# Performance work log

Hardware: AMD Instinct MI355X
Metric: run time of the kernel (lower is better)

Reference implementation:

```python
import jax, jax.numpy as jnp
import numpy as np

AUDIO_DIM, SEM_DIM, ATTN_DIM = 512, 768, 128


def setup_inputs() -> dict:
    key = jax.random.key(0)
    ks = jax.random.split(key, 12)
    B, T, T_sem = 8, 4096, 1024
    s = lambda d: 1.0 / np.sqrt(d)
    return {
        "x_ct": jax.random.normal(ks[0], (B, AUDIO_DIM, T), jnp.float32),
        "sem_btd": jax.random.normal(ks[1], (B, T_sem, SEM_DIM), jnp.float32),
        "ln_w": jnp.ones((AUDIO_DIM,), jnp.float32),
        "ln_b": jnp.zeros((AUDIO_DIM,), jnp.float32),
        "Wq": jax.random.normal(ks[2], (AUDIO_DIM, ATTN_DIM), jnp.float32) * s(AUDIO_DIM),
        "bq": jnp.zeros((ATTN_DIM,), jnp.float32),
        "Wk": jax.random.normal(ks[3], (SEM_DIM, ATTN_DIM), jnp.float32) * s(SEM_DIM),
        "bk": jnp.zeros((ATTN_DIM,), jnp.float32),
        "Wv": jax.random.normal(ks[4], (SEM_DIM, ATTN_DIM), jnp.float32) * s(SEM_DIM),
        "bv": jnp.zeros((ATTN_DIM,), jnp.float32),
        "Wo": jax.random.normal(ks[5], (ATTN_DIM, AUDIO_DIM), jnp.float32) * s(ATTN_DIM),
        "bo": jnp.zeros((AUDIO_DIM,), jnp.float32),
    }


def _layernorm(x, w, b, eps=1e-5):
    mu = jnp.mean(x, axis=-1, keepdims=True)
    var = jnp.mean(jnp.square(x - mu), axis=-1, keepdims=True)
    return (x - mu) * jax.lax.rsqrt(var + eps) * w + b


def reference(x_ct, sem_btd, ln_w, ln_b, Wq, bq, Wk, bk, Wv, bv, Wo, bo):
    # x_ct: [B, C, T] -> [B, T, C]
    x = jnp.swapaxes(x_ct, 1, 2)
    x = _layernorm(x, ln_w, ln_b)
    Q = x @ Wq + bq                      # [B, T, A]
    K = sem_btd @ Wk + bk                # [B, S, A]
    V = sem_btd @ Wv + bv                # [B, S, A]
    scale = ATTN_DIM ** -0.5
    attn = jnp.einsum("bta,bsa->bts", Q, K) * scale
    attn = jax.nn.softmax(attn, axis=-1)  # dropout: eval mode (identity)
    ctx = jnp.einsum("bts,bsa->bta", attn, V)
    delta = ctx @ Wo + bo                # [B, T, C]
    return jnp.swapaxes(delta, 1, 2)     # [B, C, T]
```

## Files before the change

### kernel.cpp

```cpp
#include <hip/hip_runtime.h>
#include <hip/hip_bf16.h>
#include <math.h>

#define BATCH 8
#define TDIM 4096
#define SDIM 1024
#define CDIM 512
#define DDIM 768
#define ADIM 128

typedef short s8v __attribute__((ext_vector_type(8)));
typedef float f4v __attribute__((ext_vector_type(4)));

__device__ __forceinline__ short f2bf(float f) {
    unsigned u = __float_as_uint(f);
    u += 0x7fffu + ((u >> 16) & 1u);
    return (short)(u >> 16);
}
__device__ __forceinline__ float bf2f(short s) {
    return __uint_as_float(((unsigned)(unsigned short)s) << 16);
}
__device__ __forceinline__ f4v mfma16(s8v a, s8v b, f4v c) {
    return __builtin_amdgcn_mfma_f32_16x16x32_bf16(a, b, c, 0, 0, 0);
}
__device__ __forceinline__ void gl_lds16(const short* g, short* l) {
    __builtin_amdgcn_global_load_lds(
        (const __attribute__((address_space(1))) unsigned int*)g,
        (__attribute__((address_space(3))) unsigned int*)l, 16, 0, 0);
}

__global__ __launch_bounds__(256) void prep_w(
    const float* __restrict__ Wq, const float* __restrict__ Wk,
    const float* __restrict__ Wv, const float* __restrict__ Wo,
    const float* __restrict__ lnw, const float* __restrict__ lnb,
    const float* __restrict__ bq,
    short* __restrict__ WqT, short* __restrict__ WkT,
    short* __restrict__ WvT, short* __restrict__ WoT,
    float* __restrict__ uq, float* __restrict__ vq)
{
    __shared__ float su[2][128], sv[2][128];
    int gid = blockIdx.x * 256 + threadIdx.x;
    {
        int k = gid >> 7, n = gid & 127;
        int idx = (k >> 6) * 8192 + n * 64 + ((((k >> 3) & 7) ^ (n & 7)) * 8) + (k & 7);
        WqT[idx] = f2bf(Wq[gid] * lnw[k]);
    }
    #pragma unroll
    for (int i = 0; i < 2; ++i) {
        int e = gid + i * 65536;
        if (e < 98304) {
            int k = e >> 7, n = e & 127;
            WkT[n * 768 + k] = f2bf(Wk[e]);
            WvT[n * 768 + k] = f2bf(Wv[e]);
        }
    }
    {
        int k = gid >> 9, c = gid & 511;
        WoT[c * 128 + k] = f2bf(Wo[gid]);
    }
    if (blockIdx.x == 255) {
        int a = threadIdx.x & 127, half = threadIdx.x >> 7;
        float s1 = 0.f, s2 = 0.f;
        #pragma unroll 8
        for (int c = half * 256; c < half * 256 + 256; ++c) {
            float wv = Wq[c * 128 + a];
            s1 += bf2f(f2bf(lnw[c] * wv));
            s2 += lnb[c] * wv;
        }
        su[half][a] = s1; sv[half][a] = s2;
        __syncthreads();
        if (threadIdx.x < 128) {
            uq[a] = su[0][a] + su[1][a];
            vq[a] = sv[0][a] + sv[1][a] + bq[a];
        }
    }
}

__global__ __launch_bounds__(256) void kv_proj(
    const float* __restrict__ sem,
    const short* __restrict__ WkT, const float* __restrict__ bk,
    const short* __restrict__ WvT, const float* __restrict__ bv,
    short* __restrict__ Kb, short* __restrict__ Vb)
{
    __shared__ __align__(16) short sA[32 * 40];
    __shared__ __align__(16) short sW[2][128 * 40];
    const int tid = threadIdx.x, lane = tid & 63, wave = tid >> 6;
    const int ln15 = lane & 15, q = lane >> 4, kq = q * 8;
    const int r0 = blockIdx.x * 32;
    const int b = r0 >> 10, sbase = r0 & 1023;
    const int kv = wave >> 1;
    const int mh = wave & 1;
    const int m  = mh * 16 + ln15;

    f4v acc[8];
    #pragma unroll
    for (int j = 0; j < 8; ++j) acc[j] = (f4v)0.0f;

    const int srow = tid >> 3;
    const int sk4  = (tid & 7) * 4;

    for (int kc = 0; kc < DDIM / 32; ++kc) {
        __syncthreads();
        {
            float4 f = *(const float4*)&sem[(size_t)(r0 + srow) * DDIM + kc * 32 + sk4];
            uint2 pk;
            pk.x = (unsigned short)f2bf(f.x) | ((unsigned)(unsigned short)f2bf(f.y) << 16);
            pk.y = (unsigned short)f2bf(f.z) | ((unsigned)(unsigned short)f2bf(f.w) << 16);
            *(uint2*)&sA[srow * 40 + sk4] = pk;
        }
        #pragma unroll
        for (int i = 0; i < 2; ++i) {
            int idx8 = i * 256 + tid;
            int n = idx8 >> 2, k8 = (idx8 & 3) * 8;
            *(s8v*)&sW[0][n * 40 + k8] = *(const s8v*)&WkT[(size_t)n * 768 + kc * 32 + k8];
            *(s8v*)&sW[1][n * 40 + k8] = *(const s8v*)&WvT[(size_t)n * 768 + kc * 32 + k8];
        }
        __syncthreads();
        s8v a = *(const s8v*)&sA[m * 40 + kq];
        #pragma unroll
        for (int j = 0; j < 8; ++j) {
            s8v bb = *(const s8v*)&sW[kv][(j * 16 + ln15) * 40 + kq];
            acc[j] = mfma16(a, bb, acc[j]);
        }
    }
    const int s_in_b = sbase + mh * 16 + q * 4;
    if (kv == 0) {
        #pragma unroll
        for (int j = 0; j < 8; ++j) {
            int col = j * 16 + ln15;
            float bias = bk[col];
            #pragma unroll
            for (int r = 0; r < 4; ++r)
                Kb[((size_t)b * SDIM + s_in_b + r) * ADIM + col] = f2bf(acc[j][r] + bias);
        }
    } else {
        #pragma unroll
        for (int j = 0; j < 8; ++j) {
            int col = j * 16 + ln15;
            float bias = bv[col];
            uint2 pk;
            pk.x = (unsigned short)f2bf(acc[j][0] + bias) | ((unsigned)(unsigned short)f2bf(acc[j][1] + bias) << 16);
            pk.y = (unsigned short)f2bf(acc[j][2] + bias) | ((unsigned)(unsigned short)f2bf(acc[j][3] + bias) << 16);
            *(uint2*)&Vb[((size_t)b * ADIM + col) * SDIM + s_in_b] = pk;
        }
    }
}

__global__ __launch_bounds__(256, 3) void ln_q(
    const float* __restrict__ x,
    const short* __restrict__ WqI, const float* __restrict__ uq,
    const float* __restrict__ vq, short* __restrict__ Qb)
{
    __shared__ __align__(16) short sX[2][32 * 72];
    __shared__ __align__(16) short sW[2][64 * 128];
    __shared__ __align__(16) float redw[4][32][2];
    const int tid = threadIdx.x, lane = tid & 63, wave = tid >> 6;
    const int ln15 = lane & 15, q = lane >> 4, kq = q * 8;
    const int b = blockIdx.x >> 7;
    const int t0 = (blockIdx.x & 127) * 32;
    const float* xb = x + (size_t)b * CDIM * TDIM + t0;

    const int cc  = tid >> 2;
    const int tlo = (tid & 3) * 4;
    const int thi = 16 + tlo;
    const int wb  = wave * 64;

    float ps1[8] = {0,0,0,0,0,0,0,0}, ps2[8] = {0,0,0,0,0,0,0,0};
    const int mh = wave & 1, jb = (wave >> 1) * 4;
    const int mrow = mh * 16 + ln15;
    f4v acc[4];
    #pragma unroll
    for (int j = 0; j < 4; ++j) acc[j] = (f4v)0.0f;

    float4 f0 = *(const float4*)&xb[(size_t)cc * TDIM + tlo];
    float4 f1 = *(const float4*)&xb[(size_t)cc * TDIM + thi];
    #pragma unroll
    for (int i = 0; i < 4; ++i) {
        int ii = i * 256 + wb;
        gl_lds16(&WqI[(size_t)(ii + lane) * 8], &sW[0][ii * 8]);
    }
    {
        float v0[4] = {f0.x, f0.y, f0.z, f0.w};
        float v1[4] = {f1.x, f1.y, f1.z, f1.w};
        #pragma unroll
        for (int jj = 0; jj < 4; ++jj) {
            ps1[jj] += v0[jj];     ps2[jj] += v0[jj] * v0[jj];
            ps1[4+jj] += v1[jj];   ps2[4+jj] += v1[jj] * v1[jj];
            sX[0][(tlo + jj) * 72 + cc] = f2bf(v0[jj]);
            sX[0][(thi + jj) * 72 + cc] = f2bf(v1[jj]);
        }
    }
    __syncthreads();

    for (int kc = 0; kc < 8; ++kc) {
        const int cur = kc & 1;
        if (kc < 7) {
            const size_t cb = (size_t)(kc + 1) * 64;
            f0 = *(const float4*)&xb[(cb + cc) * TDIM + tlo];
            f1 = *(const float4*)&xb[(cb + cc) * TDIM + thi];
            const short* wch = WqI + (size_t)(kc + 1) * 8192;
            #pragma unroll
            for (int i = 0; i < 4; ++i) {
                int ii = i * 256 + wb;
                gl_lds16(&wch[(size_t)(ii + lane) * 8], &sW[cur ^ 1][ii * 8]);
            }
        }
        #pragma unroll
        for (int kk = 0; kk < 2; ++kk) {
            s8v a = *(const s8v*)&sX[cur][mrow * 72 + kk * 32 + kq];
            #pragma unroll
            for (int j = 0; j < 4; ++j) {
                int n = (jb + j) * 16 + ln15;
                s8v bb = *(const s8v*)&sW[cur][n * 64 + (((kk * 4 + q) ^ (n & 7)) * 8)];
                acc[j] = mfma16(a, bb, acc[j]);
            }
        }
        if (kc < 7) {
            float v0[4] = {f0.x, f0.y, f0.z, f0.w};
            float v1[4] = {f1.x, f1.y, f1.z, f1.w};
            #pragma unroll
            for (int jj = 0; jj < 4; ++jj) {
                ps1[jj] += v0[jj];     ps2[jj] += v0[jj] * v0[jj];
                ps1[4+jj] += v1[jj];   ps2[4+jj] += v1[jj] * v1[jj];
                sX[cur ^ 1][(tlo + jj) * 72 + cc] = f2bf(v0[jj]);
                sX[cur ^ 1][(thi + jj) * 72 + cc] = f2bf(v1[jj]);
            }
        }
        __syncthreads();
    }

    #pragma unroll
    for (int mk = 4; mk <= 32; mk <<= 1) {
        #pragma unroll
        for (int jj = 0; jj < 8; ++jj) {
            ps1[jj] += __shfl_xor(ps1[jj], mk, 64);
            ps2[jj] += __shfl_xor(ps2[jj], mk, 64);
        }
    }
    if (lane < 4) {
        #pragma unroll
        for (int jj = 0; jj < 4; ++jj) {
            redw[wave][tlo + jj][0] = ps1[jj];
            redw[wave][tlo + jj][1] = ps2[jj];
            redw[wave][thi + jj][0] = ps1[4 + jj];
            redw[wave][thi + jj][1] = ps2[4 + jj];
        }
    }
    __syncthreads();

    float u4[4], v4[4];
    #pragma unroll
    for (int j = 0; j < 4; ++j) {
        int col = (jb + j) * 16 + ln15;
        u4[j] = uq[col]; v4[j] = vq[col];
    }
    const float scale = 0.08838834764831845f;
    #pragma unroll
    for (int r = 0; r < 4; ++r) {
        int tl = mh * 16 + q * 4 + r;
        float s1 = 0.f, s2 = 0.f;
        #pragma unroll
        for (int w = 0; w < 4; ++w) {
            float2 p = *(const float2*)&redw[w][tl][0];
            s1 += p.x; s2 += p.y;
        }
        float mu = s1 * (1.f / 512.f);
        float var = s2 * (1.f / 512.f) - mu * mu;
        float rs = rsqrtf(var + 1e-5f);
        int t = t0 + tl;
        #pragma unroll
        for (int j = 0; j < 4; ++j) {
            float qv = (rs * (acc[j][r] - mu * u4[j]) + v4[j]) * scale;
            Qb[((size_t)b * TDIM + t) * ADIM + ((jb + j) * 16 + ln15)] = f2bf(qv);
        }
    }
}

__global__ __launch_bounds__(256) void attn(
    const short* __restrict__ Qb, const short* __restrict__ Kb,
    const short* __restrict__ Vb, short* __restrict__ Cx)
{
    __shared__ __align__(16) short sK [2][64 * 128];
    __shared__ __align__(16) short sVT[2][128 * 64];
    __shared__ __align__(16) short sP [64 * 64];
    const int tid = threadIdx.x, lane = tid & 63, wave = tid >> 6;
    const int ln15 = lane & 15, q = lane >> 4, kq = q * 8;
    const int b = blockIdx.x >> 6;
    const int t0 = (blockIdx.x & 63) * 64;
    const int m = wave * 16 + ln15;

    const int krow = tid >> 4, kkb = tid & 15;
    const int varow = tid >> 3, vkb = tid & 7;

    s8v qf[4];
    {
        const short* qp = Qb + ((size_t)b * TDIM + t0 + m) * ADIM + kq;
        #pragma unroll
        for (int kc = 0; kc < 4; ++kc) qf[kc] = *(const s8v*)(qp + kc * 32);
    }
    s8v ones;
    #pragma unroll
    for (int j = 0; j < 8; ++j) ones[j] = (short)0x3F80;

    f4v accO[8]; f4v accL = (f4v)0.0f;
    #pragma unroll
    for (int j = 0; j < 8; ++j) accO[j] = (f4v)0.0f;

    const short* Kbase = Kb + (size_t)b * SDIM * ADIM;
    const short* Vbase = Vb + (size_t)b * ADIM * SDIM;
    s8v rk[4], rv[4];

    #pragma unroll
    for (int i = 0; i < 4; ++i) {
        rk[i] = *(const s8v*)(Kbase + (size_t)(i * 16 + krow) * ADIM + kkb * 8);
        rv[i] = *(const s8v*)(Vbase + (size_t)(i * 32 + varow) * SDIM + vkb * 8);
    }
    #pragma unroll
    for (int i = 0; i < 4; ++i) {
        int r = i * 16 + krow;
        *(s8v*)&sK[0][r * 128 + ((kkb ^ (r & 15)) * 8)] = rk[i];
        int a = i * 32 + varow;
        *(s8v*)&sVT[0][a * 64 + ((vkb ^ (a & 7)) * 8)] = rv[i];
    }
    __syncthreads();

    for (int sc = 0; sc < SDIM / 64; ++sc) {
        const int cur = sc & 1;
        if (sc < 15) {
            const int s0n = (sc + 1) * 64;
            #pragma unroll
            for (int i = 0; i < 4; ++i) {
                rk[i] = *(const s8v*)(Kbase + (size_t)(s0n + i * 16 + krow) * ADIM + kkb * 8);
                rv[i] = *(const s8v*)(Vbase + (size_t)(i * 32 + varow) * SDIM + s0n + vkb * 8);
            }
        }
        #pragma unroll
        for (int j = 0; j < 4; ++j) {
            f4v sacc = (f4v)0.0f;
            const int row = j * 16 + ln15;
            #pragma unroll
            for (int kc = 0; kc < 4; ++kc) {
                s8v bb = *(const s8v*)&sK[cur][row * 128 + (((kc * 4 + q) ^ (row & 15)) * 8)];
                sacc = mfma16(qf[kc], bb, sacc);
            }
            #pragma unroll
            for (int r = 0; r < 4; ++r) {
                float ev = __expf(sacc[r]);
                int prow = wave * 16 + q * 4 + r;
                int pcol = j * 16 + ln15;
                sP[prow * 64 + (((pcol >> 3) ^ (prow & 7)) * 8) + (pcol & 7)] = f2bf(ev);
            }
        }
        #pragma unroll
        for (int kc = 0; kc < 2; ++kc) {
            s8v pa = *(const s8v*)&sP[m * 64 + (((kc * 4 + q) ^ (m & 7)) * 8)];
            accL = mfma16(pa, ones, accL);
            #pragma unroll
            for (int j = 0; j < 8; ++j) {
                int a = j * 16 + ln15;
                s8v bb = *(const s8v*)&sVT[cur][a * 64 + (((kc * 4 + q) ^ (a & 7)) * 8)];
                accO[j] = mfma16(pa, bb, accO[j]);
            }
        }
        if (sc < 15) {
            #pragma unroll
            for (int i = 0; i < 4; ++i) {
                int r = i * 16 + krow;
                *(s8v*)&sK[cur ^ 1][r * 128 + ((kkb ^ (r & 15)) * 8)] = rk[i];
                int a = i * 32 + varow;
                *(s8v*)&sVT[cur ^ 1][a * 64 + ((vkb ^ (a & 7)) * 8)] = rv[i];
            }
        }
        __syncthreads();
    }
    #pragma unroll
    for (int r = 0; r < 4; ++r) {
        float rinv = 1.0f / accL[r];
        int t = t0 + wave * 16 + q * 4 + r;
        #pragma unroll
        for (int j = 0; j < 8; ++j) {
            int col = j * 16 + ln15;
            Cx[((size_t)b * TDIM + t) * ADIM + col] = f2bf(accO[j][r] * rinv);
        }
    }
}

__global__ __launch_bounds__(256) void out_proj(
    const short* __restrict__ Cx, const short* __restrict__ WoT,
    const float* __restrict__ bo, float* __restrict__ out)
{
    __shared__ __align__(16) short sCtx[64 * 136];
    __shared__ __align__(16) char  buf[128 * 136 * 2];
    short* sWoT = (short*)buf;
    float* outT = (float*)buf;
    const int tid = threadIdx.x, lane = tid & 63, wave = tid >> 6;
    const int ln15 = lane & 15, q = lane >> 4, kq = q * 8;
    const int b = blockIdx.x >> 8;
    const int rem = blockIdx.x & 255;
    const int t0 = (rem & 63) * 64;
    const int c0 = (rem >> 6) * 128;

    #pragma unroll
    for (int i = 0; i < 4; ++i) {
        int idx8 = i * 256 + tid;
        int row = idx8 >> 4, a8 = (idx8 & 15) * 8;
        *(s8v*)&sCtx[row * 136 + a8] = *(const s8v*)&Cx[((size_t)b * TDIM + t0 + row) * ADIM + a8];
    }
    #pragma unroll
    for (int i = 0; i < 8; ++i) {
        int idx8 = i * 256 + tid;
        int n = idx8 >> 4, k8 = (idx8 & 15) * 8;
        *(s8v*)&sWoT[n * 136 + k8] = *(const s8v*)&WoT[(size_t)(c0 + n) * ADIM + k8];
    }
    __syncthreads();
    f4v acc[8];
    #pragma unroll
    for (int j = 0; j < 8; ++j) acc[j] = (f4v)0.0f;
    const int m = wave * 16 + ln15;
    #pragma unroll
    for (int kc = 0; kc < 4; ++kc) {
        s8v a = *(const s8v*)&sCtx[m * 136 + kc * 32 + kq];
        #pragma unroll
        for (int j = 0; j < 8; ++j) {
            s8v bb = *(const s8v*)&sWoT[(j * 16 + ln15) * 136 + kc * 32 + kq];
            acc[j] = mfma16(a, bb, acc[j]);
        }
    }
    __syncthreads();
    #pragma unroll
    for (int j = 0; j < 8; ++j) {
        int cl = j * 16 + ln15;
        float bias = bo[c0 + cl];
        #pragma unroll
        for (int r = 0; r < 4; ++r) {
            int tl = wave * 16 + q * 4 + r;
            outT[cl * 68 + tl] = acc[j][r] + bias;
        }
    }
    __syncthreads();
    #pragma unroll
    for (int i = 0; i < 8; ++i) {
        int idx4 = i * 256 + tid;
        int c = idx4 >> 4, t4 = (idx4 & 15) * 4;
        float4 v = *(const float4*)&outT[c * 68 + t4];
        *(float4*)&out[((size_t)b * CDIM + c0 + c) * TDIM + t0 + t4] = v;
    }
}

extern "C" void kernel_launch(void* const* d_in, const int* in_sizes, int n_in,
                              void* d_out, int out_size, void* d_ws, size_t ws_size,
                              hipStream_t stream) {
    const float* x   = (const float*)d_in[0];
    const float* sem = (const float*)d_in[1];
    const float* lnw = (const float*)d_in[2];
    const float* lnb = (const float*)d_in[3];
    const float* Wq  = (const float*)d_in[4];
    const float* bq  = (const float*)d_in[5];
    const float* Wk  = (const float*)d_in[6];
    const float* bk  = (const float*)d_in[7];
    const float* Wv  = (const float*)d_in[8];
    const float* bv  = (const float*)d_in[9];
    const float* Wo  = (const float*)d_in[10];
    const float* bo  = (const float*)d_in[11];
    float* out = (float*)d_out;

    short* ws  = (short*)d_ws;
    short* Qb  = ws;
    short* Kb  = Qb  + (size_t)BATCH * TDIM * ADIM;
    short* Vb  = Kb  + (size_t)BATCH * SDIM * ADIM;
    short* Cx  = Vb  + (size_t)BATCH * SDIM * ADIM;
    short* WqT = Cx  + (size_t)BATCH * TDIM * ADIM;
    short* WkT = WqT + 128 * 512;
    short* WvT = WkT + 128 * 768;
    short* WoT = WvT + 128 * 768;
    float* uq  = (float*)(WoT + 512 * 128);
    float* vq  = uq + 128;

    hipLaunchKernelGGL(prep_w,  dim3(256),  dim3(256), 0, stream,
                       Wq, Wk, Wv, Wo, lnw, lnb, bq, WqT, WkT, WvT, WoT, uq, vq);
    hipLaunchKernelGGL(kv_proj, dim3(256),  dim3(256), 0, stream, sem, WkT, bk, WvT, bv, Kb, Vb);
    hipLaunchKernelGGL(ln_q,    dim3(1024), dim3(256), 0, stream, x, WqT, uq, vq, Qb);
    hipLaunchKernelGGL(attn,    dim3(512),  dim3(256), 0, stream, Qb, Kb, Vb, Cx);
    hipLaunchKernelGGL(out_proj,dim3(2048), dim3(256), 0, stream, Cx, WoT, bo, out);
}
```

Baseline: 250.1 us.

## Enlarge LN+Q tile to 128 rows and parallelize uq/vq reduction with atomics

The LayerNorm+Q projection kernel now runs 512-thread blocks over 128 time steps. Each wave computes all 128 output columns, so every staged Wq chunk is reused by four times as many rows. The x loads are coalesced along T, and rows are paired across half-waves with shuffles to write XOR-swizzled bf16 tiles into LDS. Separately, the serial per-column reduction for uq/vq is moved out of a single prep_w block into a new 256-block kernel that accumulates with atomicAdd, removing a long single-block tail. In exchange there is one extra kernel launch, nondeterministic float summation order, and fewer, larger ln_q blocks with more LDS per block.

After: 241.5 us. -3.4%, faster.

```diff
diff --git a/kernel.cpp b/kernel.cpp
--- a/kernel.cpp
+++ b/kernel.cpp
@@ -32,14 +32,13 @@
 __global__ __launch_bounds__(256) void prep_w(
     const float* __restrict__ Wq, const float* __restrict__ Wk,
     const float* __restrict__ Wv, const float* __restrict__ Wo,
-    const float* __restrict__ lnw, const float* __restrict__ lnb,
-    const float* __restrict__ bq,
+    const float* __restrict__ lnw,
     short* __restrict__ WqT, short* __restrict__ WkT,
     short* __restrict__ WvT, short* __restrict__ WoT,
-    float* __restrict__ uq, float* __restrict__ vq)
-{
-    __shared__ float su[2][128], sv[2][128];
+    float* __restrict__ uq)
+{
     int gid = blockIdx.x * 256 + threadIdx.x;
+    if (blockIdx.x == 0) uq[threadIdx.x] = 0.f;
     {
         int k = gid >> 7, n = gid & 127;
         int idx = (k >> 6) * 8192 + n * 64 + ((((k >> 3) & 7) ^ (n & 7)) * 8) + (k & 7);
@@ -58,21 +57,24 @@
         int k = gid >> 9, c = gid & 511;
         WoT[c * 128 + k] = f2bf(Wo[gid]);
     }
-    if (blockIdx.x == 255) {
-        int a = threadIdx.x & 127, half = threadIdx.x >> 7;
-        float s1 = 0.f, s2 = 0.f;
-        #pragma unroll 8
-        for (int c = half * 256; c < half * 256 + 256; ++c) {
-            float wv = Wq[c * 128 + a];
-            s1 += bf2f(f2bf(lnw[c] * wv));
-            s2 += lnb[c] * wv;
-        }
-        su[half][a] = s1; sv[half][a] = s2;
-        __syncthreads();
-        if (threadIdx.x < 128) {
-            uq[a] = su[0][a] + su[1][a];
-            vq[a] = sv[0][a] + sv[1][a] + bq[a];
-        }
+}
+
+__global__ __launch_bounds__(256) void prep_uv(
+    const float* __restrict__ Wq, const float* __restrict__ lnw,
+    const float* __restrict__ lnb,
+    float* __restrict__ uq, float* __restrict__ vq)
+{
+    __shared__ float r1[128], r2[128];
+    const int a = threadIdx.x & 127, h = threadIdx.x >> 7;
+    const int c = blockIdx.x * 2 + h;
+    float wv = Wq[c * 128 + a];
+    float s1 = bf2f(f2bf(lnw[c] * wv));
+    float s2 = lnb[c] * wv;
+    if (h) { r1[a] = s1; r2[a] = s2; }
+    __syncthreads();
+    if (!h) {
+        atomicAdd(&uq[a], s1 + r1[a]);
+        atomicAdd(&vq[a], s2 + r2[a]);
     }
 }
 
@@ -146,134 +148,140 @@
     }
 }
 
-__global__ __launch_bounds__(256, 3) void ln_q(
+__global__ __launch_bounds__(512) void ln_q(
     const float* __restrict__ x,
     const short* __restrict__ WqI, const float* __restrict__ uq,
-    const float* __restrict__ vq, short* __restrict__ Qb)
-{
-    __shared__ __align__(16) short sX[2][32 * 72];
+    const float* __restrict__ vq, const float* __restrict__ bq,
+    short* __restrict__ Qb)
+{
+    __shared__ __align__(16) short sX[2][128 * 72];
     __shared__ __align__(16) short sW[2][64 * 128];
-    __shared__ __align__(16) float redw[4][32][2];
+    __shared__ __align__(16) float redw[8][32][4][2];
     const int tid = threadIdx.x, lane = tid & 63, wave = tid >> 6;
     const int ln15 = lane & 15, q = lane >> 4, kq = q * 8;
-    const int b = blockIdx.x >> 7;
-    const int t0 = (blockIdx.x & 127) * 32;
+    const int b = blockIdx.x >> 5;
+    const int t0 = (blockIdx.x & 31) * 128;
     const float* xb = x + (size_t)b * CDIM * TDIM + t0;
 
-    const int cc  = tid >> 2;
-    const int tlo = (tid & 3) * 4;
-    const int thi = 16 + tlo;
-    const int wb  = wave * 64;
-
-    float ps1[8] = {0,0,0,0,0,0,0,0}, ps2[8] = {0,0,0,0,0,0,0,0};
-    const int mh = wave & 1, jb = (wave >> 1) * 4;
-    const int mrow = mh * 16 + ln15;
-    f4v acc[4];
-    #pragma unroll
-    for (int j = 0; j < 4; ++j) acc[j] = (f4v)0.0f;
-
-    float4 f0 = *(const float4*)&xb[(size_t)cc * TDIM + tlo];
-    float4 f1 = *(const float4*)&xb[(size_t)cc * TDIM + thi];
-    #pragma unroll
-    for (int i = 0; i < 4; ++i) {
-        int ii = i * 256 + wb;
-        gl_lds16(&WqI[(size_t)(ii + lane) * 8], &sW[0][ii * 8]);
-    }
-    {
-        float v0[4] = {f0.x, f0.y, f0.z, f0.w};
-        float v1[4] = {f1.x, f1.y, f1.z, f1.w};
-        #pragma unroll
-        for (int jj = 0; jj < 4; ++jj) {
-            ps1[jj] += v0[jj];     ps2[jj] += v0[jj] * v0[jj];
-            ps1[4+jj] += v1[jj];   ps2[4+jj] += v1[jj] * v1[jj];
-            sX[0][(tlo + jj) * 72 + cc] = f2bf(v0[jj]);
-            sX[0][(thi + jj) * 72 + cc] = f2bf(v1[jj]);
-        }
-    }
+    const int l5 = lane >> 5;
+    const int tq = (lane & 31) * 4;
+    const int cw = wave * 2 + l5;
+
+    float ps1[4] = {0.f,0.f,0.f,0.f}, ps2[4] = {0.f,0.f,0.f,0.f};
+    const int m = wave * 16 + ln15;
+    const int swzm = m & 7;
+    f4v acc[8];
+    #pragma unroll
+    for (int j = 0; j < 8; ++j) acc[j] = (f4v)0.0f;
+
+    float4 xv[4];
+
+#define PROC_X(BUF) do {                                                      \
+    _Pragma("unroll")                                                         \
+    for (int i = 0; i < 4; ++i) {                                             \
+        float4 v = xv[i];                                                     \
+        ps1[0] += v.x; ps2[0] += v.x * v.x;                                   \
+        ps1[1] += v.y; ps2[1] += v.y * v.y;                                   \
+        ps1[2] += v.z; ps2[2] += v.z * v.z;                                   \
+        ps1[3] += v.w; ps2[3] += v.w * v.w;                                   \
+        float o0 = __shfl_xor(v.x, 32); float o1 = __shfl_xor(v.y, 32);       \
+        float o2 = __shfl_xor(v.z, 32); float o3 = __shfl_xor(v.w, 32);       \
+        const int ccE = i * 16 + wave * 2;                                    \
+        unsigned wA, wB; int tA, tB;                                          \
+        if (l5 == 0) {                                                        \
+            tA = tq; tB = tq + 1;                                             \
+            wA = (unsigned short)f2bf(v.x) | ((unsigned)(unsigned short)f2bf(o0) << 16); \
+            wB = (unsigned short)f2bf(v.y) | ((unsigned)(unsigned short)f2bf(o1) << 16); \
+        } else {                                                              \
+            tA = tq + 2; tB = tq + 3;                                         \
+            wA = (unsigned short)f2bf(o2) | ((unsigned)(unsigned short)f2bf(v.z) << 16); \
+            wB = (unsigned short)f2bf(o3) | ((unsigned)(unsigned short)f2bf(v.w) << 16); \
+        }                                                                     \
+        *(unsigned*)&sX[BUF][tA * 72 + (((ccE >> 3) ^ (tA & 7)) * 8) + (ccE & 7)] = wA; \
+        *(unsigned*)&sX[BUF][tB * 72 + (((ccE >> 3) ^ (tB & 7)) * 8) + (ccE & 7)] = wB; \
+    }                                                                         \
+} while (0)
+
+    #pragma unroll
+    for (int i = 0; i < 4; ++i)
+        xv[i] = *(const float4*)&xb[(size_t)(i * 16 + cw) * TDIM + tq];
+    #pragma unroll
+    for (int i = 0; i < 2; ++i) {
+        int gi = i * 512 + wave * 64;
+        gl_lds16(&WqI[(size_t)(gi + lane) * 8], &sW[0][gi * 8]);
+    }
+    PROC_X(0);
     __syncthreads();
 
     for (int kc = 0; kc < 8; ++kc) {
         const int cur = kc & 1;
         if (kc < 7) {
-            const size_t cb = (size_t)(kc + 1) * 64;
-            f0 = *(const float4*)&xb[(cb + cc) * TDIM + tlo];
-            f1 = *(const float4*)&xb[(cb + cc) * TDIM + thi];
+            const float* xc = xb + (size_t)(kc + 1) * 64 * TDIM;
+            #pragma unroll
+            for (int i = 0; i < 4; ++i)
+                xv[i] = *(const float4*)&xc[(size_t)(i * 16 + cw) * TDIM + tq];
             const short* wch = WqI + (size_t)(kc + 1) * 8192;
             #pragma unroll
-            for (int i = 0; i < 4; ++i) {
-                int ii = i * 256 + wb;
-                gl_lds16(&wch[(size_t)(ii + lane) * 8], &sW[cur ^ 1][ii * 8]);
+            for (int i = 0; i < 2; ++i) {
+                int gi = i * 512 + wave * 64;
+                gl_lds16(&wch[(size_t)(gi + lane) * 8], &sW[cur ^ 1][gi * 8]);
             }
         }
         #pragma unroll
         for (int kk = 0; kk < 2; ++kk) {
-            s8v a = *(const s8v*)&sX[cur][mrow * 72 + kk * 32 + kq];
-            #pragma unroll
-            for (int j = 0; j < 4; ++j) {
-                int n = (jb + j) * 16 + ln15;
+            s8v a = *(const s8v*)&sX[cur][m * 72 + (((kk * 4 + q) ^ swzm) * 8)];
+            #pragma unroll
+            for (int j = 0; j < 8; ++j) {
+                int n = j * 16 + ln15;
                 s8v bb = *(const s8v*)&sW[cur][n * 64 + (((kk * 4 + q) ^ (n & 7)) * 8)];
                 acc[j] = mfma16(a, bb, acc[j]);
             }
         }
-        if (kc < 7) {
-            float v0[4] = {f0.x, f0.y, f0.z, f0.w};
-            float v1[4] = {f1.x, f1.y, f1.z, f1.w};
-            #pragma unroll
-            for (int jj = 0; jj < 4; ++jj) {
-                ps1[jj] += v0[jj];     ps2[jj] += v0[jj] * v0[jj];
-                ps1[4+jj] += v1[jj];   ps2[4+jj] += v1[jj] * v1[jj];
-                sX[cur ^ 1][(tlo + jj) * 72 + cc] = f2bf(v0[jj]);
-                sX[cur ^ 1][(thi + jj) * 72 + cc] = f2bf(v1[jj]);
-            }
-        }
+        if (kc < 7) PROC_X(cur ^ 1);
         __syncthreads();
     }
 
     #pragma unroll
-    for (int mk = 4; mk <= 32; mk <<= 1) {
-        #pragma unroll
-        for (int jj = 0; jj < 8; ++jj) {
-            ps1[jj] += __shfl_xor(ps1[jj], mk, 64);
-            ps2[jj] += __shfl_xor(ps2[jj], mk, 64);
-        }
-    }
-    if (lane < 4) {
+    for (int jj = 0; jj < 4; ++jj) {
+        ps1[jj] += __shfl_xor(ps1[jj], 32);
+        ps2[jj] += __shfl_xor(ps2[jj], 32);
+    }
+    if (lane < 32) {
         #pragma unroll
         for (int jj = 0; jj < 4; ++jj) {
-            redw[wave][tlo + jj][0] = ps1[jj];
-            redw[wave][tlo + jj][1] = ps2[jj];
-            redw[wave][thi + jj][0] = ps1[4 + jj];
-            redw[wave][thi + jj][1] = ps2[4 + jj];
-        }
-    }
-    __syncthreads();
-
-    float u4[4], v4[4];
-    #pragma unroll
-    for (int j = 0; j < 4; ++j) {
-        int col = (jb + j) * 16 + ln15;
-        u4[j] = uq[col]; v4[j] = vq[col];
+            redw[wave][lane][jj][0] = ps1[jj];
+            redw[wave][lane][jj][1] = ps2[jj];
+        }
+    }
+    __syncthreads();
+
+    float u4[8], v4[8];
+    #pragma unroll
+    for (int j = 0; j < 8; ++j) {
+        int col = j * 16 + ln15;
+        u4[j] = uq[col]; v4[j] = vq[col] + bq[col];
     }
     const float scale = 0.08838834764831845f;
+    const int quad = wave * 4 + q;
     #pragma unroll
     for (int r = 0; r < 4; ++r) {
-        int tl = mh * 16 + q * 4 + r;
         float s1 = 0.f, s2 = 0.f;
         #pragma unroll
-        for (int w = 0; w < 4; ++w) {
-            float2 p = *(const float2*)&redw[w][tl][0];
+        for (int w = 0; w < 8; ++w) {
+            float2 p = *(const float2*)&redw[w][quad][r][0];
             s1 += p.x; s2 += p.y;
         }
         float mu = s1 * (1.f / 512.f);
         float var = s2 * (1.f / 512.f) - mu * mu;
         float rs = rsqrtf(var + 1e-5f);
-        int t = t0 + tl;
-        #pragma unroll
-        for (int j = 0; j < 4; ++j) {
+        int t = t0 + wave * 16 + q * 4 + r;
+        #pragma unroll
+        for (int j = 0; j < 8; ++j) {
             float qv = (rs * (acc[j][r] - mu * u4[j]) + v4[j]) * scale;
-            Qb[((size_t)b * TDIM + t) * ADIM + ((jb + j) * 16 + ln15)] = f2bf(qv);
-        }
-    }
+            Qb[((size_t)b * TDIM + t) * ADIM + (j * 16 + ln15)] = f2bf(qv);
+        }
+    }
+#undef PROC_X
 }
 
 __global__ __launch_bounds__(256) void attn(
@@ -477,9 +485,10 @@
     float* vq  = uq + 128;
 
     hipLaunchKernelGGL(prep_w,  dim3(256),  dim3(256), 0, stream,
-                       Wq, Wk, Wv, Wo, lnw, lnb, bq, WqT, WkT, WvT, WoT, uq, vq);
+                       Wq, Wk, Wv, Wo, lnw, WqT, WkT, WvT, WoT, uq);
+    hipLaunchKernelGGL(prep_uv, dim3(256),  dim3(256), 0, stream, Wq, lnw, lnb, uq, vq);
     hipLaunchKernelGGL(kv_proj, dim3(256),  dim3(256), 0, stream, sem, WkT, bk, WvT, bv, Kb, Vb);
-    hipLaunchKernelGGL(ln_q,    dim3(1024), dim3(256), 0, stream, x, WqT, uq, vq, Qb);
+    hipLaunchKernelGGL(ln_q,    dim3(256),  dim3(512), 0, stream, x, WqT, uq, vq, bq, Qb);
     hipLaunchKernelGGL(attn,    dim3(512),  dim3(256), 0, stream, Qb, Kb, Vb, Cx);
     hipLaunchKernelGGL(out_proj,dim3(2048), dim3(256), 0, stream, Cx, WoT, bo, out);
 }
```
